# Performance work log

Hardware: AMD Instinct MI355X
Metric: run time of the kernel (lower is better)

Reference implementation:

```python
import jax, jax.numpy as jnp
import numpy as np

V, E, H, L, MAXLEN, B = 32000, 512, 512, 2, 99, 4096

def setup_inputs() -> dict:
    key = jax.random.key(0)
    ks = jax.random.split(key, 16)
    s = 0.02
    return {
        "inputs": jax.random.randint(ks[0], (B, 1), 0, V),
        "hidden": jax.random.normal(ks[1], (L, B, H), dtype=jnp.float32),
        "encoder_outputs": jax.random.normal(ks[2], (B, MAXLEN, H), dtype=jnp.float32),
        "embedding": jax.random.normal(ks[3], (V, E), dtype=jnp.float32) * s,
        "attn_W": jax.random.normal(ks[4], (MAXLEN, 2 * H), dtype=jnp.float32) * s,
        "attn_b": jnp.zeros((MAXLEN,), jnp.float32),
        "combine_W": jax.random.normal(ks[5], (H, 2 * H), dtype=jnp.float32) * s,
        "combine_b": jnp.zeros((H,), jnp.float32),
        "W_ih": jax.random.normal(ks[6], (L, 3 * H, H), dtype=jnp.float32) * s,
        "W_hh": jax.random.normal(ks[7], (L, 3 * H, H), dtype=jnp.float32) * s,
        "b_ih": jnp.zeros((L, 3 * H), jnp.float32),
        "b_hh": jnp.zeros((L, 3 * H), jnp.float32),
        "out_W": jax.random.normal(ks[8], (V, H), dtype=jnp.float32) * s,
        "out_b": jnp.zeros((V,), jnp.float32),
    }

def reference(inputs, hidden, encoder_outputs, embedding, attn_W, attn_b,
              combine_W, combine_b, W_ih, W_hh, b_ih, b_hh, out_W, out_b):
    # embedding lookup (dropout is identity in eval)
    emb = embedding[inputs[:, 0]]                                   # [B, E]
    # Bahdanau-style attention over encoder outputs
    q = jnp.concatenate([emb, hidden[0]], axis=1)                   # [B, 2H]
    attn_weights = jax.nn.softmax(q @ attn_W.T + attn_b, axis=1)    # [B, max_len]
    attn_applied = jnp.einsum('bl,blh->bh', attn_weights, encoder_outputs)  # [B, H]
    x = jax.nn.relu(jnp.concatenate([emb, attn_applied], axis=1) @ combine_W.T + combine_b)  # [B, H]
    # single-step multi-layer GRU (PyTorch gate math)
    n_layers = hidden.shape[0]
    new_h = []
    inp = x
    for l in range(n_layers):  # small fixed structural loop
        h = hidden[l]
        gi = inp @ W_ih[l].T + b_ih[l]
        gh = h @ W_hh[l].T + b_hh[l]
        i_r, i_z, i_n = jnp.split(gi, 3, axis=1)
        h_r, h_z, h_n = jnp.split(gh, 3, axis=1)
        r = jax.nn.sigmoid(i_r + h_r)
        z = jax.nn.sigmoid(i_z + h_z)
        n = jnp.tanh(i_n + r * h_n)
        h_new = (1.0 - z) * n + z * h
        new_h.append(h_new)
        inp = h_new
    hidden_new = jnp.stack(new_h)                                   # [L, B, H]
    pred = jax.nn.softmax(inp @ out_W.T + out_b, axis=1)            # [B, V]
    return pred, hidden_new, attn_weights
```

## Files before the change

kernel.cpp:

```cpp
#include <hip/hip_runtime.h>
#include <cstdint>
#include <cstddef>
#include <cmath>

#define B 4096
#define H 512
#define E 512
#define V 32000
#define NL 2
#define MAXLEN 99

typedef __attribute__((ext_vector_type(8))) short  bf16x8;
typedef __attribute__((ext_vector_type(4))) float  f32x4;
typedef __attribute__((ext_vector_type(8))) unsigned short ushort8;

__device__ __forceinline__ unsigned short f2b(float x) {
    union { float f; unsigned u; } c; c.f = x;
    unsigned r = c.u + 0x7fff + ((c.u >> 16) & 1);
    return (unsigned short)(r >> 16);
}
__device__ __forceinline__ float b2f(unsigned short u) {
    return __uint_as_float((unsigned)u << 16);
}

#define GLOAD16(gp, lp)                                                        \
    __builtin_amdgcn_global_load_lds(                                          \
        (const __attribute__((address_space(1))) void*)(gp),                   \
        (__attribute__((address_space(3))) void*)(lp), 16, 0, 0)

__global__ __launch_bounds__(256) void embed_attn_kernel(
    const int* __restrict__ tok, const float* __restrict__ emb,
    const float* __restrict__ hidden0, const float* __restrict__ attn_W,
    const float* __restrict__ attn_b, const float* __restrict__ enc,
    float* __restrict__ attnw, unsigned short* __restrict__ c2b)
{
    const int b = blockIdx.x, t = threadIdx.x;
    __shared__ float qs[1024];
    __shared__ float ls[128];

    const int v = tok[b];
    const float2 e = ((const float2*)(emb + (size_t)v * E))[t];
    qs[2 * t] = e.x; qs[2 * t + 1] = e.y;
    ushort2 eb; eb.x = f2b(e.x); eb.y = f2b(e.y);
    *(ushort2*)&c2b[(size_t)b * 1024 + 2 * t] = eb;
    const float2 h = ((const float2*)(hidden0 + (size_t)b * H))[t];
    qs[512 + 2 * t] = h.x; qs[512 + 2 * t + 1] = h.y;
    __syncthreads();

    float s = -1e30f;
    if (t < MAXLEN) {
        const float4* w4 = (const float4*)(attn_W + (size_t)t * 1024);
        const float4* q4 = (const float4*)qs;
        float ax = 0.f, ay = 0.f, az = 0.f, aw = 0.f;
        #pragma unroll 8
        for (int k = 0; k < 256; ++k) {
            const float4 a = q4[k], w = w4[k];
            ax += a.x * w.x; ay += a.y * w.y; az += a.z * w.z; aw += a.w * w.w;
        }
        s = (ax + ay) + (az + aw) + attn_b[t];
    }
    if (t < 128) ls[t] = s;
    __syncthreads();

    float mx = -1e30f;
    for (int i = 0; i < 128; ++i) mx = fmaxf(mx, ls[i]);
    __syncthreads();

    float ex = 0.f;
    if (t < MAXLEN) ex = expf(s - mx);
    if (t < 128) ls[t] = ex;
    __syncthreads();

    float sum = 0.f;
    for (int i = 0; i < 128; ++i) sum += ls[i];
    const float inv = 1.0f / sum;

    if (t < MAXLEN) attnw[(size_t)b * MAXLEN + t] = ex * inv;

    float accx = 0.f, accy = 0.f;
    const float2* encb = (const float2*)(enc + (size_t)b * MAXLEN * H);
    for (int l = 0; l < MAXLEN; ++l) {
        const float wl = ls[l];
        const float2 ev = encb[(size_t)l * 256 + t];
        accx += wl * ev.x; accy += wl * ev.y;
    }
    ushort2 ab; ab.x = f2b(accx * inv); ab.y = f2b(accy * inv);
    *(ushort2*)&c2b[(size_t)b * 1024 + 512 + 2 * t] = ab;
}

__global__ __launch_bounds__(256) void batch_f2b_kernel(
    const float* __restrict__ s0, unsigned short* __restrict__ d0, int e0,
    const float* __restrict__ s1, unsigned short* __restrict__ d1, int e1,
    const float* __restrict__ s2, unsigned short* __restrict__ d2, int e2,
    const float* __restrict__ s3, unsigned short* __restrict__ d3, int e3,
    const float* __restrict__ s4, unsigned short* __restrict__ d4)
{
    int blk = blockIdx.x;
    const float* s; unsigned short* d;
    if      (blk < e0) { s = s0; d = d0; }
    else if (blk < e1) { s = s1; d = d1; blk -= e0; }
    else if (blk < e2) { s = s2; d = d2; blk -= e1; }
    else if (blk < e3) { s = s3; d = d3; blk -= e2; }
    else               { s = s4; d = d4; blk -= e3; }
    const size_t i = ((size_t)blk * 256 + threadIdx.x) * 8;
    const float4 a = *(const float4*)(s + i);
    const float4 b = *(const float4*)(s + i + 4);
    ushort8 o;
    o[0] = f2b(a.x); o[1] = f2b(a.y); o[2] = f2b(a.z); o[3] = f2b(a.w);
    o[4] = f2b(b.x); o[5] = f2b(b.y); o[6] = f2b(b.z); o[7] = f2b(b.w);
    *(ushort8*)(d + i) = o;
}

template<int RELU, int OUTBF, int PARTIALS>
__device__ __forceinline__ void gemm_core(
    const unsigned short* __restrict__ A, const unsigned short* __restrict__ Wb,
    const float* __restrict__ bias, void* __restrict__ Cv,
    int M, int N, int K, int ldc, int colOff,
    float* __restrict__ pmax_g, float* __restrict__ psum_g, int bm, int bn)
{
    __shared__ __align__(16) unsigned short As[2][4096];
    __shared__ __align__(16) unsigned short Bs[2][4096];

    const int tid  = threadIdx.x;
    const int lane = tid & 63;
    const int wid  = tid >> 6;
    const int wr   = (wid >> 1) * 64;
    const int wc   = (wid & 1) * 64;
    const int fr   = lane & 15;
    const int fk   = (lane >> 4) * 8;

    f32x4 acc[4][4];
    #pragma unroll
    for (int m = 0; m < 4; ++m)
        #pragma unroll
        for (int n = 0; n < 4; ++n) acc[m][n] = (f32x4)0.f;

    const int srow = tid >> 2;
    const int sk   = (tid & 3) * 8;

    const unsigned short* ga = A  + (size_t)(bm + srow) * K + sk;
    const unsigned short* gb = Wb + (size_t)(bn + srow) * K + sk;

    {
        GLOAD16(ga,                    &As[0][tid * 8]);
        GLOAD16(ga + (size_t)64 * K,   &As[0][2048 + tid * 8]);
        GLOAD16(gb,                    &Bs[0][tid * 8]);
        GLOAD16(gb + (size_t)64 * K,   &Bs[0][2048 + tid * 8]);
    }

    int buf = 0;
    for (int k0 = 0; k0 < K; k0 += 32) {
        __syncthreads();

        if (k0 + 32 < K) {
            const int nb = buf ^ 1;
            GLOAD16(ga + k0 + 32,                  &As[nb][tid * 8]);
            GLOAD16(ga + k0 + 32 + (size_t)64 * K, &As[nb][2048 + tid * 8]);
            GLOAD16(gb + k0 + 32,                  &Bs[nb][tid * 8]);
            GLOAD16(gb + k0 + 32 + (size_t)64 * K, &Bs[nb][2048 + tid * 8]);
        }

        bf16x8 af[4], bf_[4];
        #pragma unroll
        for (int m = 0; m < 4; ++m)
            af[m] = *(const bf16x8*)&As[buf][(wr + m * 16 + fr) * 32 + fk];
        #pragma unroll
        for (int n = 0; n < 4; ++n)
            bf_[n] = *(const bf16x8*)&Bs[buf][(wc + n * 16 + fr) * 32 + fk];

        #pragma unroll
        for (int m = 0; m < 4; ++m)
            #pragma unroll
            for (int n = 0; n < 4; ++n)
                acc[m][n] = __builtin_amdgcn_mfma_f32_16x16x32_bf16(
                    af[m], bf_[n], acc[m][n], 0, 0, 0);

        buf ^= 1;
    }

    float bv[4];
    #pragma unroll
    for (int n = 0; n < 4; ++n) bv[n] = bias[bn + wc + n * 16 + fr];

    if constexpr (PARTIALS) {
        __shared__ float pm_s[2][2][64];
        __shared__ float ps_s[2][2][64];
        const int wrIdx = wid >> 1, wcIdx = wid & 1;

        #pragma unroll
        for (int m = 0; m < 4; ++m) {
            #pragma unroll
            for (int r = 0; r < 4; ++r) {
                float vmax = -1e30f;
                #pragma unroll
                for (int n = 0; n < 4; ++n) vmax = fmaxf(vmax, acc[m][n][r] + bv[n]);
                vmax = fmaxf(vmax, __shfl_xor(vmax, 1));
                vmax = fmaxf(vmax, __shfl_xor(vmax, 2));
                vmax = fmaxf(vmax, __shfl_xor(vmax, 4));
                vmax = fmaxf(vmax, __shfl_xor(vmax, 8));
                float vsum = 0.f;
                #pragma unroll
                for (int n = 0; n < 4; ++n) vsum += expf(acc[m][n][r] + bv[n] - vmax);
                vsum += __shfl_xor(vsum, 1);
                vsum += __shfl_xor(vsum, 2);
                vsum += __shfl_xor(vsum, 4);
                vsum += __shfl_xor(vsum, 8);
                const int rowh = m * 16 + (lane >> 4) * 4 + r;
                if (fr == 0) { pm_s[wrIdx][wcIdx][rowh] = vmax; ps_s[wrIdx][wcIdx][rowh] = vsum; }
            }
        }
        __syncthreads();
        if (wcIdx == 0) {
            const float m0 = pm_s[wrIdx][0][lane], m1 = pm_s[wrIdx][1][lane];
            const float s0 = ps_s[wrIdx][0][lane], s1 = ps_s[wrIdx][1][lane];
            const float Mx = fmaxf(m0, m1);
            const float S  = s0 * expf(m0 - Mx) + s1 * expf(m1 - Mx);
            const int row = bm + wr + lane;
            const int nt  = bn >> 7;
            const int NT  = N >> 7;
            pmax_g[(size_t)row * NT + nt] = Mx;
            psum_g[(size_t)row * NT + nt] = S;
        }
    }

    if constexpr (OUTBF) {
        __syncthreads();
        unsigned short* smb = (wr == 0) ? (unsigned short*)As : (unsigned short*)Bs;
        #pragma unroll
        for (int m = 0; m < 4; ++m) {
            #pragma unroll
            for (int n = 0; n < 4; ++n) {
                #pragma unroll
                for (int r = 0; r < 4; ++r) {
                    float v = acc[m][n][r] + bv[n];
                    if (RELU) v = fmaxf(v, 0.f);
                    const int row  = m * 16 + (lane >> 4) * 4 + r;
                    const int col  = wc + n * 16 + fr;
                    const int cc   = col ^ ((row & 12) << 3);
                    smb[row * 128 + cc] = f2b(v);
                }
            }
        }
        __syncthreads();
        unsigned short* Cb = (unsigned short*)Cv;
        const int rrow = tid >> 4;
        const int cch  = (tid & 15) * 8;
        #pragma unroll
        for (int p = 0; p < 8; ++p) {
            const int row  = p * 16 + rrow;
            const int lrow = row & 63;
            unsigned short* smr = (p < 4) ? (unsigned short*)As : (unsigned short*)Bs;
            const int cc = cch ^ ((row & 12) << 3);
            const ushort8 v = *(const ushort8*)&smr[lrow * 128 + cc];
            *(ushort8*)&Cb[(size_t)(bm + row) * ldc + colOff + bn + cch] = v;
        }
    } else {
        float* Cf = (float*)Cv;
        #pragma unroll
        for (int m = 0; m < 4; ++m) {
            #pragma unroll
            for (int n = 0; n < 4; ++n) {
                const int col = bn + wc + n * 16 + fr;
                const int row = bm + wr + m * 16 + (lane >> 4) * 4;
                #pragma unroll
                for (int r = 0; r < 4; ++r) {
                    float v = acc[m][n][r] + bv[n];
                    if (RELU) v = fmaxf(v, 0.f);
                    Cf[(size_t)(row + r) * ldc + colOff + col] = v;
                }
            }
        }
    }
}

template<int RELU, int OUTBF, int PARTIALS, int GSWAP>
__global__ __launch_bounds__(256) void gemm_bf16_nt(
    const unsigned short* __restrict__ A, const unsigned short* __restrict__ Wb,
    const float* __restrict__ bias, void* __restrict__ Cv,
    int M, int N, int K, int ldc, int colOff,
    float* __restrict__ pmax_g, float* __restrict__ psum_g)
{
    int bm, bn;
    if (GSWAP == 2) {
        const int orig = blockIdx.x;
        const int q8   = gridDim.x >> 3;
        const int id   = (orig & 7) * q8 + (orig >> 3);
        const int mt   = M >> 7;
        bm = (id % mt) * 128;
        bn = (id / mt) * 128;
    } else if (GSWAP == 1) {
        bn = blockIdx.y * 128;
        bm = blockIdx.x * 128;
    } else {
        bn = blockIdx.x * 128;
        bm = blockIdx.y * 128;
    }
    gemm_core<RELU, OUTBF, PARTIALS>(A, Wb, bias, Cv, M, N, K, ldc, colOff,
                                     pmax_g, psum_g, bm, bn);
}

__global__ __launch_bounds__(256) void gemm_bf16_dual(
    const unsigned short* __restrict__ A0, const unsigned short* __restrict__ W0,
    const float* __restrict__ b0, void* __restrict__ C0,
    const unsigned short* __restrict__ A1, const unsigned short* __restrict__ W1,
    const float* __restrict__ b1, void* __restrict__ C1,
    int M, int N, int K, int ldc)
{
    const int bn = blockIdx.x * 128;
    const int bm = blockIdx.y * 128;
    const unsigned short* A = blockIdx.z ? A1 : A0;
    const unsigned short* W = blockIdx.z ? W1 : W0;
    const float* bias       = blockIdx.z ? b1 : b0;
    void* C                 = blockIdx.z ? C1 : C0;
    gemm_core<0, 1, 0>(A, W, bias, C, M, N, K, ldc, 0, nullptr, nullptr, bm, bn);
}

template<int RELU>
__global__ __launch_bounds__(256) void gemm_nt(
    const float* __restrict__ A, const float* __restrict__ W,
    const float* __restrict__ bias, float* __restrict__ C,
    int M, int N, int K)
{
    constexpr int BM = 128, BN = 128, BK = 32;
    __shared__ float As[BK][BM + 4];
    __shared__ float Bs[BK][BN + 4];

    const int tid = threadIdx.x;
    const int bn = blockIdx.x * BN;
    const int bm = blockIdx.y * BM;
    const int tx = tid & 15;
    const int ty = tid >> 4;

    float acc[8][8];
    #pragma unroll
    for (int i = 0; i < 8; ++i)
        #pragma unroll
        for (int j = 0; j < 8; ++j) acc[i][j] = 0.f;

    const int lkv = tid & 7;
    const int lm0 = tid >> 3;

    for (int k0 = 0; k0 < K; k0 += BK) {
        #pragma unroll
        for (int r = 0; r < 4; ++r) {
            const int m = lm0 + 32 * r;
            const float4 va = *(const float4*)(A + (size_t)(bm + m) * K + k0 + lkv * 4);
            As[lkv * 4 + 0][m] = va.x; As[lkv * 4 + 1][m] = va.y;
            As[lkv * 4 + 2][m] = va.z; As[lkv * 4 + 3][m] = va.w;
            const float4 vb = *(const float4*)(W + (size_t)(bn + m) * K + k0 + lkv * 4);
            Bs[lkv * 4 + 0][m] = vb.x; Bs[lkv * 4 + 1][m] = vb.y;
            Bs[lkv * 4 + 2][m] = vb.z; Bs[lkv * 4 + 3][m] = vb.w;
        }
        __syncthreads();

        #pragma unroll
        for (int kk = 0; kk < BK; ++kk) {
            float a[8], bb[8];
            *(float4*)&a[0]  = *(const float4*)&As[kk][ty * 8];
            *(float4*)&a[4]  = *(const float4*)&As[kk][ty * 8 + 4];
            *(float4*)&bb[0] = *(const float4*)&Bs[kk][tx * 8];
            *(float4*)&bb[4] = *(const float4*)&Bs[kk][tx * 8 + 4];
            #pragma unroll
            for (int i = 0; i < 8; ++i)
                #pragma unroll
                for (int j = 0; j < 8; ++j) acc[i][j] += a[i] * bb[j];
        }
        __syncthreads();
    }

    #pragma unroll
    for (int i = 0; i < 8; ++i) {
        const int row = bm + ty * 8 + i;
        float* crow = C + (size_t)row * N + bn + tx * 8;
        #pragma unroll
        for (int j = 0; j < 8; ++j) {
            float v = acc[i][j] + bias[bn + tx * 8 + j];
            if (RELU) v = fmaxf(v, 0.f);
            crow[j] = v;
        }
    }
}

__global__ __launch_bounds__(256) void gru_gates_kernel(
    const unsigned short* __restrict__ gi, const unsigned short* __restrict__ gh,
    const float* __restrict__ h, float* __restrict__ hnew,
    unsigned short* __restrict__ hnew_b)
{
    const int idx = blockIdx.x * 256 + threadIdx.x;
    const int b  = idx >> 6;
    const int j8 = (idx & 63) * 8;
    const size_t base = (size_t)b * 1536;
    const ushort8 vir = *(const ushort8*)&gi[base + j8];
    const ushort8 viz = *(const ushort8*)&gi[base + 512 + j8];
    const ushort8 vin = *(const ushort8*)&gi[base + 1024 + j8];
    const ushort8 vhr = *(const ushort8*)&gh[base + j8];
    const ushort8 vhz = *(const ushort8*)&gh[base + 512 + j8];
    const ushort8 vhn = *(const ushort8*)&gh[base + 1024 + j8];
    const size_t hi = (size_t)b * 512 + j8;
    const float4 h0 = *(const float4*)&h[hi];
    const float4 h1 = *(const float4*)&h[hi + 4];
    const float hval[8] = {h0.x, h0.y, h0.z, h0.w, h1.x, h1.y, h1.z, h1.w};
    float hv[8];
    ushort8 ob;
    #pragma unroll
    for (int k = 0; k < 8; ++k) {
        const float r = 1.f / (1.f + expf(-(b2f(vir[k]) + b2f(vhr[k]))));
        const float z = 1.f / (1.f + expf(-(b2f(viz[k]) + b2f(vhz[k]))));
        const float n = tanhf(b2f(vin[k]) + r * b2f(vhn[k]));
        hv[k] = (1.f - z) * n + z * hval[k];
        ob[k] = f2b(hv[k]);
    }
    float4 o0, o1;
    o0.x = hv[0]; o0.y = hv[1]; o0.z = hv[2]; o0.w = hv[3];
    o1.x = hv[4]; o1.y = hv[5]; o1.z = hv[6]; o1.w = hv[7];
    *(float4*)&hnew[hi]     = o0;
    *(float4*)&hnew[hi + 4] = o1;
    *(ushort8*)&hnew_b[hi]  = ob;
}

__global__ __launch_bounds__(256) void softmax_apply_stats_kernel(
    float* logits, const float* __restrict__ pmax,
    const float* __restrict__ psum, int NT)
{
    const int row = blockIdx.x, t = threadIdx.x;
    __shared__ float redM[256], redS[256];

    float Mx = -1e30f, S = 0.f;
    for (int i = t; i < NT; i += 256) {
        const float m = pmax[(size_t)row * NT + i];
        const float s = psum[(size_t)row * NT + i];
        const float nm = fmaxf(Mx, m);
        S = S * expf(Mx - nm) + s * expf(m - nm);
        Mx = nm;
    }
    redM[t] = Mx; redS[t] = S;
    __syncthreads();
    for (int st = 128; st > 0; st >>= 1) {
        if (t < st) {
            const float m2 = redM[t + st], s2 = redS[t + st];
            const float nm = fmaxf(redM[t], m2);
            redS[t] = redS[t] * expf(redM[t] - nm) + s2 * expf(m2 - nm);
            redM[t] = nm;
        }
        __syncthreads();
    }
    const float MxF = redM[0];
    const float is  = 1.f / redS[0];

    const unsigned short* src = (const unsigned short*)logits + (size_t)row * (2 * V) + V;
    ushort8 buf[16];
    #pragma unroll
    for (int k = 0; k < 16; ++k) {
        const int i = t + 256 * k;
        if (i < V / 8) buf[k] = *(const ushort8*)&src[i * 8];
    }
    __syncthreads();
    float* dst = logits + (size_t)row * V;
    #pragma unroll
    for (int k = 0; k < 16; ++k) {
        const int i = t + 256 * k;
        if (i < V / 8) {
            float4 o0, o1;
            o0.x = expf(b2f(buf[k][0]) - MxF) * is;
            o0.y = expf(b2f(buf[k][1]) - MxF) * is;
            o0.z = expf(b2f(buf[k][2]) - MxF) * is;
            o0.w = expf(b2f(buf[k][3]) - MxF) * is;
            o1.x = expf(b2f(buf[k][4]) - MxF) * is;
            o1.y = expf(b2f(buf[k][5]) - MxF) * is;
            o1.z = expf(b2f(buf[k][6]) - MxF) * is;
            o1.w = expf(b2f(buf[k][7]) - MxF) * is;
            *(float4*)&dst[i * 8]     = o0;
            *(float4*)&dst[i * 8 + 4] = o1;
        }
    }
}

__global__ __launch_bounds__(256) void softmax_rows_kernel(float* __restrict__ logits, int N)
{
    const int b = blockIdx.x, t = threadIdx.x;
    __shared__ float red[256];
    float* row = logits + (size_t)b * N;

    float mx = -1e30f;
    for (int i = t; i < N; i += 256) mx = fmaxf(mx, row[i]);
    red[t] = mx; __syncthreads();
    for (int s = 128; s > 0; s >>= 1) { if (t < s) red[t] = fmaxf(red[t], red[t + s]); __syncthreads(); }
    mx = red[0]; __syncthreads();

    float sum = 0.f;
    for (int i = t; i < N; i += 256) sum += expf(row[i] - mx);
    red[t] = sum; __syncthreads();
    for (int s = 128; s > 0; s >>= 1) { if (t < s) red[t] += red[t + s]; __syncthreads(); }
    const float inv = 1.0f / red[0];
    __syncthreads();

    for (int i = t; i < N; i += 256) row[i] = expf(row[i] - mx) * inv;
}

extern "C" void kernel_launch(void* const* d_in, const int* in_sizes, int n_in,
                              void* d_out, int out_size, void* d_ws, size_t ws_size,
                              hipStream_t stream)
{
    const int*   tok    = (const int*)d_in[0];
    const float* hidden = (const float*)d_in[1];
    const float* enc    = (const float*)d_in[2];
    const float* emb    = (const float*)d_in[3];
    const float* attn_W = (const float*)d_in[4];
    const float* attn_b = (const float*)d_in[5];
    const float* comb_W = (const float*)d_in[6];
    const float* comb_b = (const float*)d_in[7];
    const float* W_ih   = (const float*)d_in[8];
    const float* W_hh   = (const float*)d_in[9];
    const float* b_ih   = (const float*)d_in[10];
    const float* b_hh   = (const float*)d_in[11];
    const float* out_W  = (const float*)d_in[12];
    const float* out_b  = (const float*)d_in[13];

    float* out   = (float*)d_out;
    float* pred  = out;
    float* hid_o = out + (size_t)B * V;
    float* attnw = hid_o + (size_t)NL * B * H;

    unsigned short* c2b    = (unsigned short*)pred;
    unsigned short* xb     = c2b  + (size_t)B * 1024;
    unsigned short* h01b   = xb   + (size_t)B * 512;
    unsigned short* hn0b   = h01b + (size_t)NL * B * 512;
    unsigned short* gi_b   = hn0b + (size_t)B * 512;
    unsigned short* gh_b   = gi_b + (size_t)B * 1536;
    unsigned short* Wihb   = gh_b + (size_t)B * 1536;
    unsigned short* Whhb   = Wihb + (size_t)NL * 1536 * 512;
    unsigned short* combWb = Whhb + (size_t)NL * 1536 * 512;
    unsigned short* hn1b_fallback = combWb + (size_t)512 * 1024;

    const size_t outWb_e = (size_t)V * H;
    const size_t hn1b_e  = (size_t)B * H;
    const int    NT      = V / 128;
    const size_t bf_bytes = (outWb_e + hn1b_e) * sizeof(unsigned short);
    const size_t pt_bytes = ((size_t)B * NT * 2 + 2 * B) * sizeof(float);
    const bool lvl1 = ws_size >= bf_bytes;
    const bool lvl2 = ws_size >= bf_bytes + pt_bytes;

    unsigned short* outWb = (unsigned short*)d_ws;
    unsigned short* hn1b  = lvl1 ? outWb + outWb_e : hn1b_fallback;
    float* pmax_g  = (float*)((char*)d_ws + bf_bytes);
    float* psum_g  = pmax_g + (size_t)B * NT;

    unsigned short* h0b = h01b;
    unsigned short* h1b = h01b + (size_t)B * 512;

    embed_attn_kernel<<<B, 256, 0, stream>>>(
        tok, emb, hidden, attn_W, attn_b, enc, attnw, c2b);

    {
        const int e0 = 256, e1 = e0 + 768, e2 = e1 + 768, e3 = e2 + 2048;
        const int nblk = lvl1 ? e3 + 8000 : e3;
        batch_f2b_kernel<<<nblk, 256, 0, stream>>>(
            comb_W, combWb, e0,
            W_ih,   Wihb,   e1,
            W_hh,   Whhb,   e2,
            hidden, h01b,   e3,
            out_W,  outWb);
    }

    gemm_bf16_nt<1, 1, 0, 0><<<dim3(512 / 128, B / 128), 256, 0, stream>>>(
        c2b, combWb, comb_b, xb, B, 512, 1024, 512, 0, nullptr, nullptr);

    gemm_bf16_dual<<<dim3(1536 / 128, B / 128, 2), 256, 0, stream>>>(
        xb,  Wihb, b_ih, gi_b,
        h0b, Whhb, b_hh, gh_b, B, 1536, 512, 1536);
    gru_gates_kernel<<<(B * H / 8) / 256, 256, 0, stream>>>(
        gi_b, gh_b, hidden, hid_o, hn0b);

    gemm_bf16_dual<<<dim3(1536 / 128, B / 128, 2), 256, 0, stream>>>(
        hn0b, Wihb + (size_t)1536 * 512, b_ih + 1536, gi_b,
        h1b,  Whhb + (size_t)1536 * 512, b_hh + 1536, gh_b, B, 1536, 512, 1536);
    gru_gates_kernel<<<(B * H / 8) / 256, 256, 0, stream>>>(
        gi_b, gh_b, hidden + (size_t)B * H, hid_o + (size_t)B * H, hn1b);

    if (lvl2) {
        gemm_bf16_nt<0, 1, 1, 2><<<(B / 128) * (V / 128), 256, 0, stream>>>(
            hn1b, outWb, out_b, pred, B, V, 512, 2 * V, V, pmax_g, psum_g);
        softmax_apply_stats_kernel<<<B, 256, 0, stream>>>(pred, pmax_g, psum_g, NT);
    } else if (lvl1) {
        gemm_bf16_nt<0, 0, 0, 1><<<dim3(B / 128, V / 128), 256, 0, stream>>>(
            hn1b, outWb, out_b, pred, B, V, 512, V, 0, nullptr, nullptr);
        softmax_rows_kernel<<<B, 256, 0, stream>>>(pred, V);
    } else {
        gemm_nt<0><<<dim3(V / 128, B / 128), 256, 0, stream>>>(
            hid_o + (size_t)B * H, out_W, out_b, pred, B, V, 512);
        softmax_rows_kernel<<<B, 256, 0, stream>>>(pred, V);
    }
}
```

Baseline: 899.0 us.

## Fuse attention and weight-conversion launches; specialize logits GEMM with higher occupancy

Merges the embedding/attention kernel and the fp32-to-bf16 weight conversion kernel into one launch, with extra blocks doing the conversion, so the two independent workloads share the GPU and one launch is removed. Adds a dedicated logits GEMM kernel with compile-time shapes and launch_bounds(256,5), and reuses the As shared buffer for the softmax partial statistics so LDS use drops and more blocks fit per CU. The grid swizzle for the logits GEMM is replaced by a plain 2D grid with M-major ordering. Risks are register pressure from the occupancy bound and worse L2 reuse without the swizzle.

```diff
diff --git a/kernel.cpp b/kernel.cpp
--- a/kernel.cpp
+++ b/kernel.cpp
@@ -28,16 +28,40 @@
         (const __attribute__((address_space(1))) void*)(gp),                   \
         (__attribute__((address_space(3))) void*)(lp), 16, 0, 0)
 
-__global__ __launch_bounds__(256) void embed_attn_kernel(
+__global__ __launch_bounds__(256) void embed_attn_f2b_kernel(
     const int* __restrict__ tok, const float* __restrict__ emb,
     const float* __restrict__ hidden0, const float* __restrict__ attn_W,
     const float* __restrict__ attn_b, const float* __restrict__ enc,
-    float* __restrict__ attnw, unsigned short* __restrict__ c2b)
-{
-    const int b = blockIdx.x, t = threadIdx.x;
+    float* __restrict__ attnw, unsigned short* __restrict__ c2b,
+    const float* __restrict__ s0, unsigned short* __restrict__ d0, int e0,
+    const float* __restrict__ s1, unsigned short* __restrict__ d1, int e1,
+    const float* __restrict__ s2, unsigned short* __restrict__ d2, int e2,
+    const float* __restrict__ s3, unsigned short* __restrict__ d3, int e3,
+    const float* __restrict__ s4, unsigned short* __restrict__ d4)
+{
     __shared__ float qs[1024];
     __shared__ float ls[128];
-
+    const int t = threadIdx.x;
+
+    if ((int)blockIdx.x >= B) {
+        int blk = blockIdx.x - B;
+        const float* s; unsigned short* d;
+        if      (blk < e0) { s = s0; d = d0; }
+        else if (blk < e1) { s = s1; d = d1; blk -= e0; }
+        else if (blk < e2) { s = s2; d = d2; blk -= e1; }
+        else if (blk < e3) { s = s3; d = d3; blk -= e2; }
+        else               { s = s4; d = d4; blk -= e3; }
+        const size_t i = ((size_t)blk * 256 + t) * 8;
+        const float4 a = *(const float4*)(s + i);
+        const float4 b = *(const float4*)(s + i + 4);
+        ushort8 o;
+        o[0] = f2b(a.x); o[1] = f2b(a.y); o[2] = f2b(a.z); o[3] = f2b(a.w);
+        o[4] = f2b(b.x); o[5] = f2b(b.y); o[6] = f2b(b.z); o[7] = f2b(b.w);
+        *(ushort8*)(d + i) = o;
+        return;
+    }
+
+    const int b = blockIdx.x;
     const int v = tok[b];
     const float2 e = ((const float2*)(emb + (size_t)v * E))[t];
     qs[2 * t] = e.x; qs[2 * t + 1] = e.y;
@@ -88,29 +112,6 @@
     *(ushort2*)&c2b[(size_t)b * 1024 + 512 + 2 * t] = ab;
 }
 
-__global__ __launch_bounds__(256) void batch_f2b_kernel(
-    const float* __restrict__ s0, unsigned short* __restrict__ d0, int e0,
-    const float* __restrict__ s1, unsigned short* __restrict__ d1, int e1,
-    const float* __restrict__ s2, unsigned short* __restrict__ d2, int e2,
-    const float* __restrict__ s3, unsigned short* __restrict__ d3, int e3,
-    const float* __restrict__ s4, unsigned short* __restrict__ d4)
-{
-    int blk = blockIdx.x;
-    const float* s; unsigned short* d;
-    if      (blk < e0) { s = s0; d = d0; }
-    else if (blk < e1) { s = s1; d = d1; blk -= e0; }
-    else if (blk < e2) { s = s2; d = d2; blk -= e1; }
-    else if (blk < e3) { s = s3; d = d3; blk -= e2; }
-    else               { s = s4; d = d4; blk -= e3; }
-    const size_t i = ((size_t)blk * 256 + threadIdx.x) * 8;
-    const float4 a = *(const float4*)(s + i);
-    const float4 b = *(const float4*)(s + i + 4);
-    ushort8 o;
-    o[0] = f2b(a.x); o[1] = f2b(a.y); o[2] = f2b(a.z); o[3] = f2b(a.w);
-    o[4] = f2b(b.x); o[5] = f2b(b.y); o[6] = f2b(b.z); o[7] = f2b(b.w);
-    *(ushort8*)(d + i) = o;
-}
-
 template<int RELU, int OUTBF, int PARTIALS>
 __device__ __forceinline__ void gemm_core(
     const unsigned short* __restrict__ A, const unsigned short* __restrict__ Wb,
@@ -183,9 +184,10 @@
     for (int n = 0; n < 4; ++n) bv[n] = bias[bn + wc + n * 16 + fr];
 
     if constexpr (PARTIALS) {
-        __shared__ float pm_s[2][2][64];
-        __shared__ float ps_s[2][2][64];
+        float* pm_s = (float*)&As[0][0];
+        float* ps_s = pm_s + 256;
         const int wrIdx = wid >> 1, wcIdx = wid & 1;
+        const int seg = (wrIdx * 2 + wcIdx) * 64;
 
         #pragma unroll
         for (int m = 0; m < 4; ++m) {
@@ -206,13 +208,15 @@
                 vsum += __shfl_xor(vsum, 4);
                 vsum += __shfl_xor(vsum, 8);
                 const int rowh = m * 16 + (lane >> 4) * 4 + r;
-                if (fr == 0) { pm_s[wrIdx][wcIdx][rowh] = vmax; ps_s[wrIdx][wcIdx][rowh] = vsum; }
+                if (fr == 0) { pm_s[seg + rowh] = vmax; ps_s[seg + rowh] = vsum; }
             }
         }
         __syncthreads();
         if (wcIdx == 0) {
-            const float m0 = pm_s[wrIdx][0][lane], m1 = pm_s[wrIdx][1][lane];
-            const float s0 = ps_s[wrIdx][0][lane], s1 = ps_s[wrIdx][1][lane];
+            const float m0 = pm_s[(wrIdx * 2 + 0) * 64 + lane];
+            const float m1 = pm_s[(wrIdx * 2 + 1) * 64 + lane];
+            const float s0 = ps_s[(wrIdx * 2 + 0) * 64 + lane];
+            const float s1 = ps_s[(wrIdx * 2 + 1) * 64 + lane];
             const float Mx = fmaxf(m0, m1);
             const float S  = s0 * expf(m0 - Mx) + s1 * expf(m1 - Mx);
             const int row = bm + wr + lane;
@@ -280,23 +284,21 @@
     int M, int N, int K, int ldc, int colOff,
     float* __restrict__ pmax_g, float* __restrict__ psum_g)
 {
-    int bm, bn;
-    if (GSWAP == 2) {
-        const int orig = blockIdx.x;
-        const int q8   = gridDim.x >> 3;
-        const int id   = (orig & 7) * q8 + (orig >> 3);
-        const int mt   = M >> 7;
-        bm = (id % mt) * 128;
-        bn = (id / mt) * 128;
-    } else if (GSWAP == 1) {
-        bn = blockIdx.y * 128;
-        bm = blockIdx.x * 128;
-    } else {
-        bn = blockIdx.x * 128;
-        bm = blockIdx.y * 128;
-    }
+    const int bn = (GSWAP ? blockIdx.y : blockIdx.x) * 128;
+    const int bm = (GSWAP ? blockIdx.x : blockIdx.y) * 128;
     gemm_core<RELU, OUTBF, PARTIALS>(A, Wb, bias, Cv, M, N, K, ldc, colOff,
                                      pmax_g, psum_g, bm, bn);
+}
+
+__global__ __launch_bounds__(256, 5) void gemm_logits_kernel(
+    const unsigned short* __restrict__ A, const unsigned short* __restrict__ Wb,
+    const float* __restrict__ bias, void* __restrict__ Cv,
+    float* __restrict__ pmax_g, float* __restrict__ psum_g)
+{
+    const int bm = blockIdx.x * 128;
+    const int bn = blockIdx.y * 128;
+    gemm_core<0, 1, 1>(A, Wb, bias, Cv, B, V, 512, 2 * V, V,
+                       pmax_g, psum_g, bm, bn);
 }
 
 __global__ __launch_bounds__(256) void gemm_bf16_dual(
@@ -548,13 +550,11 @@
     unsigned short* h0b = h01b;
     unsigned short* h1b = h01b + (size_t)B * 512;
 
-    embed_attn_kernel<<<B, 256, 0, stream>>>(
-        tok, emb, hidden, attn_W, attn_b, enc, attnw, c2b);
-
     {
         const int e0 = 256, e1 = e0 + 768, e2 = e1 + 768, e3 = e2 + 2048;
-        const int nblk = lvl1 ? e3 + 8000 : e3;
-        batch_f2b_kernel<<<nblk, 256, 0, stream>>>(
+        const int nconv = lvl1 ? e3 + 8000 : e3;
+        embed_attn_f2b_kernel<<<B + nconv, 256, 0, stream>>>(
+            tok, emb, hidden, attn_W, attn_b, enc, attnw, c2b,
             comb_W, combWb, e0,
             W_ih,   Wihb,   e1,
             W_hh,   Whhb,   e2,
@@ -578,8 +578,8 @@
         gi_b, gh_b, hidden + (size_t)B * H, hid_o + (size_t)B * H, hn1b);
 
     if (lvl2) {
-        gemm_bf16_nt<0, 1, 1, 2><<<(B / 128) * (V / 128), 256, 0, stream>>>(
-            hn1b, outWb, out_b, pred, B, V, 512, 2 * V, V, pmax_g, psum_g);
+        gemm_logits_kernel<<<dim3(B / 128, V / 128), 256, 0, stream>>>(
+            hn1b, outWb, out_b, pred, pmax_g, psum_g);
         softmax_apply_stats_kernel<<<B, 256, 0, stream>>>(pred, pmax_g, psum_g, NT);
     } else if (lvl1) {
         gemm_bf16_nt<0, 0, 0, 1><<<dim3(B / 128, V / 128), 256, 0, stream>>>(
```

Result: slower. 971.4 us (+8.1%).
